# Kernel tuning notes

Measured on AMD Instinct MI355X. Metric: run time of the kernel, lower is better.

Reference implementation:

```python
import jax, jax.numpy as jnp
import numpy as np

B, C, H, W = 16, 512, 64, 64

def _conv1x1_relu(x, Wk, bk):
    # 1x1 conv (stride 1) + ReLU, as in the conv2d helper
    return jax.nn.relu(jnp.einsum('bchw,oc->bohw', x, Wk) + bk[None, :, None, None])

def _maxpool2(t):
    b, c, h, w = t.shape
    return t.reshape(b, c, h // 2, 2, w // 2, 2).max(axis=(3, 5))

def setup_inputs() -> dict:
    key = jax.random.key(0)
    ks = jax.random.split(key, 10)
    s = 0.05
    x = jax.random.normal(ks[0], (B, C, H, W), jnp.float32)
    W_theta = jax.random.normal(ks[1], (C // 8, C), jnp.float32) * s
    b_theta = jnp.zeros((C // 8,), jnp.float32)
    W_phi = jax.random.normal(ks[2], (C // 8, C), jnp.float32) * s
    b_phi = jnp.zeros((C // 8,), jnp.float32)
    W_g = jax.random.normal(ks[3], (C // 2, C), jnp.float32) * s
    b_g = jnp.zeros((C // 2,), jnp.float32)
    W_o = jax.random.normal(ks[4], (C, C // 2), jnp.float32) * s
    b_o = jnp.zeros((C,), jnp.float32)
    gamma = jnp.array([0.5], jnp.float32)  # nonzero so attention branch contributes
    return {"x": x, "W_theta": W_theta, "b_theta": b_theta, "W_phi": W_phi,
            "b_phi": b_phi, "W_g": W_g, "b_g": b_g, "W_o": W_o, "b_o": b_o,
            "gamma": gamma}

def reference(x, W_theta, b_theta, W_phi, b_phi, W_g, b_g, W_o, b_o, gamma):
    theta = _conv1x1_relu(x, W_theta, b_theta).reshape(B, C // 8, H * W)
    phi = _maxpool2(_conv1x1_relu(x, W_phi, b_phi)).reshape(B, C // 8, H * W // 4)
    g = _maxpool2(_conv1x1_relu(x, W_g, b_g)).reshape(B, C // 2, H * W // 4)
    # beta[b, n, m] = softmax_m(theta^T phi)
    beta = jax.nn.softmax(jnp.einsum('bcn,bcm->bnm', theta, phi), axis=-1)
    # o[b, c, n] = g @ beta^T
    o = jnp.einsum('bcm,bnm->bcn', g, beta).reshape(B, C // 2, H, W)
    o = _conv1x1_relu(o, W_o, b_o)
    return gamma[0] * o + x
```

## Files before the change

### kernel.cpp

```cpp
#include <hip/hip_runtime.h>
#include <cstdint>
#include <cstddef>

#define BB 16
#define CIN 512
#define NPIX 4096
#define C8 64
#define C2 256
#define MM 1024

using bf16x8 = __attribute__((ext_vector_type(8))) short;
using f32x4  = __attribute__((ext_vector_type(4))) float;

__device__ __forceinline__ short f2bf(float f) {
  union { float f; unsigned u; } v; v.f = f;
  unsigned r = v.u + 0x7FFFu + ((v.u >> 16) & 1u);
  return (short)(r >> 16);
}
__device__ __forceinline__ unsigned cvtpk(float lo, float hi) {
  unsigned r;
  asm("v_cvt_pk_bf16_f32 %0, %1, %2" : "=v"(r) : "v"(lo), "v"(hi));
  return r;
}
__device__ __forceinline__ bf16x8 ldg8(const short* p) {
  return *reinterpret_cast<const bf16x8*>(p);
}
__device__ __forceinline__ bf16x8 lds8(const short* p) {
  union { unsigned long long q[2]; bf16x8 v; } u;
  u.q[0] = *reinterpret_cast<const unsigned long long*>(p);
  u.q[1] = *reinterpret_cast<const unsigned long long*>(p + 4);
  return u.v;
}
#define MFMA(a, b, c) __builtin_amdgcn_mfma_f32_16x16x32_bf16(a, b, c, 0, 0, 0)
#define LOG2E 1.4426950408889634f

__global__ __launch_bounds__(256) void cast_w_k(const float* __restrict__ wa,
                                                const float* __restrict__ wb,
                                                const float* __restrict__ wc,
                                                const float* __restrict__ wd,
                                                short* __restrict__ out) {
  int i = blockIdx.x * 256 + threadIdx.x;
  float v;
  if (i < 32768) v = wa[i] * LOG2E;
  else if (i < 65536) v = wb[i - 32768];
  else if (i < 196608) v = wc[i - 65536];
  else v = wd[i - 196608];
  out[i] = f2bf(v);
}

__global__ __launch_bounds__(1024) void conv_mega_k(
    const float* __restrict__ x, const short* __restrict__ wbf,
    const float* __restrict__ bth, const float* __restrict__ bph,
    const float* __restrict__ bg,
    short* __restrict__ thetaT, short* __restrict__ phiT,
    short* __restrict__ gp) {
  __shared__ __align__(16) short xs[128][36];
  const int t = threadIdx.x, w = t >> 6, l = t & 63;
  const int lr = l & 15, quad = l >> 4;
  const int wg = w & 7, wh = w >> 3;
  const int bx = blockIdx.x, b = blockIdx.y;
  const int nbase = bx * 128;
  const float* xb = x + ((size_t)b * CIN << 12) + nbase;

  const int nl = t & 127, cg = t >> 7;

  f32x4 acc[3][4];
#pragma unroll
  for (int i = 0; i < 3; ++i)
#pragma unroll
    for (int j = 0; j < 4; ++j) acc[i][j] = (f32x4){0.f, 0.f, 0.f, 0.f};

  float pv0[2], pv1[2];
#pragma unroll
  for (int p = 0; p < 2; ++p) {
    int cl = (p * 8 + cg) * 2;
    pv0[p] = xb[((size_t)cl << 12) + nl];
    pv1[p] = xb[((size_t)(cl + 1) << 12) + nl];
  }

  for (int c0 = 0; c0 < CIN; c0 += 32) {
    bf16x8 af[3];
#pragma unroll
    for (int tt = 0; tt < 3; ++tt)
      af[tt] = ldg8(wbf + (size_t)(wg * 48 + tt * 16 + lr) * CIN + c0 + quad * 8);
    asm volatile("s_waitcnt lgkmcnt(0)" ::: "memory");
    __builtin_amdgcn_s_barrier();
#pragma unroll
    for (int p = 0; p < 2; ++p) {
      int cl = (p * 8 + cg) * 2;
      *reinterpret_cast<unsigned*>(&xs[nl][cl]) = cvtpk(pv0[p], pv1[p]);
    }
    asm volatile("s_waitcnt lgkmcnt(0)" ::: "memory");
    __builtin_amdgcn_s_barrier();
    if (c0 + 32 < CIN) {
#pragma unroll
      for (int p = 0; p < 2; ++p) {
        int cl = (p * 8 + cg) * 2;
        pv0[p] = xb[((size_t)(c0 + 32 + cl) << 12) + nl];
        pv1[p] = xb[((size_t)(c0 + 32 + cl + 1) << 12) + nl];
      }
    }
#pragma unroll
    for (int j = 0; j < 4; ++j) {
      const int gnt = (j & 1) + wh * 2 + (j >> 1) * 4;
      bf16x8 bfr = lds8(&xs[gnt * 16 + lr][quad * 8]);
#pragma unroll
      for (int tt = 0; tt < 3; ++tt)
        acc[tt][j] = MFMA(af[tt], bfr, acc[tt][j]);
    }
  }

#pragma unroll
  for (int tt = 0; tt < 3; ++tt) {
    const int ocb = wg * 48 + tt * 16;
    if (ocb < 64) {
      short* tb = thetaT + ((size_t)b << 12) * C8;
#pragma unroll
      for (int r = 0; r < 4; ++r) {
        int oc = ocb + quad * 4 + r;
        float bia = bth[oc] * LOG2E;
#pragma unroll
        for (int j = 0; j < 4; ++j) {
          const int gnt = (j & 1) + wh * 2 + (j >> 1) * 4;
          int n = nbase + gnt * 16 + lr;
          tb[(size_t)n * C8 + oc] = f2bf(fmaxf(acc[tt][j][r] + bia, 0.f));
        }
      }
    } else if (ocb < 128) {
      short* pb = phiT + ((size_t)b << 10) * C8;
#pragma unroll
      for (int r = 0; r < 4; ++r) {
        int oc = ocb - 64 + quad * 4 + r;
        float bia = bph[oc];
#pragma unroll
        for (int jj = 0; jj < 2; ++jj) {
          float va = fmaxf(acc[tt][jj][r] + bia, 0.f);
          float vb = fmaxf(acc[tt][jj + 2][r] + bia, 0.f);
          float pa = fmaxf(va, __shfl_xor(va, 1));
          float pbv = fmaxf(vb, __shfl_xor(vb, 1));
          float pool = fmaxf(pa, pbv);
          if ((l & 1) == 0) {
            int m = bx * 32 + wh * 16 + jj * 8 + (lr >> 1);
            pb[(size_t)m * C8 + oc] = f2bf(pool);
          }
        }
      }
    } else {
      short* gb = gp + ((size_t)b << 10) * C2;
#pragma unroll
      for (int r = 0; r < 4; ++r) {
        int oc = ocb - 128 + quad * 4 + r;
        float bia = bg[oc];
#pragma unroll
        for (int jj = 0; jj < 2; ++jj) {
          float va = fmaxf(acc[tt][jj][r] + bia, 0.f);
          float vb = fmaxf(acc[tt][jj + 2][r] + bia, 0.f);
          float pa = fmaxf(va, __shfl_xor(va, 1));
          float pbv = fmaxf(vb, __shfl_xor(vb, 1));
          float pool = fmaxf(pa, pbv);
          if ((l & 1) == 0) {
            int m = bx * 32 + wh * 16 + jj * 8 + (lr >> 1);
            gb[(size_t)oc * MM + m] = f2bf(pool);
          }
        }
      }
    }
  }
}

__global__ __launch_bounds__(256, 2) void attn_k(
    const short* __restrict__ thetaT, const short* __restrict__ phiT,
    const short* __restrict__ gp, const short* __restrict__ wo,
    const float* __restrict__ bo, const float* __restrict__ x,
    const float* __restrict__ gamma, float* __restrict__ out) {
  __shared__ __align__(16) short smem[16896];
  __shared__ float balpha[2][4][16];
  __shared__ float binv[4][16];
  const int t = threadIdx.x, w = t >> 6, l = t & 63;
  const int lr = l & 15, quad = l >> 4;
  const int blk = blockIdx.x;
  const int b = ((blk & 7) << 1) | ((blk >> 3) & 1);
  const int q0 = (blk >> 4) << 6;
  const int nw = q0 + w * 16;

  const short* thb = thetaT + ((size_t)b << 12) * C8;
  const short* phb = phiT + ((size_t)b << 10) * C8;
  const short* gpb = gp + ((size_t)b << 10) * C2;

  bf16x8 tb0 = ldg8(thb + (size_t)(nw + lr) * C8 + quad * 8);
  bf16x8 tb1 = ldg8(thb + (size_t)(nw + lr) * C8 + 32 + quad * 8);

  f32x4 oacc[4][4];
#pragma unroll
  for (int i = 0; i < 4; ++i)
#pragma unroll
    for (int j = 0; j < 4; ++j) oacc[i][j] = (f32x4){0.f, 0.f, 0.f, 0.f};
  float mrun = -3e38f, ssum = 0.f;

  auto scores = [&](int ch) {
    const int m0 = ch * 128, buf = ch & 1;
    bf16x8 ph0[8], ph1[8];
#pragma unroll
    for (int mt = 0; mt < 8; ++mt) {
      const short* pr = phb + (size_t)(m0 + mt * 16 + lr) * C8 + quad * 8;
      ph0[mt] = ldg8(pr);
      ph1[mt] = ldg8(pr + 32);
    }
    f32x4 sacc[8];
#pragma unroll
    for (int i = 0; i < 8; ++i) sacc[i] = (f32x4){0.f, 0.f, 0.f, 0.f};
#pragma unroll
    for (int mt = 0; mt < 8; ++mt) {
      sacc[mt] = MFMA(ph0[mt], tb0, sacc[mt]);
      sacc[mt] = MFMA(ph1[mt], tb1, sacc[mt]);
    }
    float cmax = sacc[0][0];
#pragma unroll
    for (int mt = 0; mt < 8; ++mt)
      cmax = fmaxf(cmax, fmaxf(fmaxf(sacc[mt][0], sacc[mt][1]),
                               fmaxf(sacc[mt][2], sacc[mt][3])));
    cmax = fmaxf(cmax, __shfl_xor(cmax, 16));
    cmax = fmaxf(cmax, __shfl_xor(cmax, 32));
    const float mnew = fmaxf(mrun, cmax);
    const float al = exp2f(mrun - mnew);
    mrun = mnew;
    float rsum = 0.f;
    short* prow = smem + ((((buf << 2) | w) << 4) + lr) * 132;
#pragma unroll
    for (int mt = 0; mt < 8; ++mt) {
      float e0 = exp2f(sacc[mt][0] - mnew);
      float e1 = exp2f(sacc[mt][1] - mnew);
      float e2 = exp2f(sacc[mt][2] - mnew);
      float e3 = exp2f(sacc[mt][3] - mnew);
      rsum += (e0 + e1) + (e2 + e3);
      uint2 pk2;
      pk2.x = cvtpk(e0, e1);
      pk2.y = cvtpk(e2, e3);
      *reinterpret_cast<uint2*>(prow + mt * 16 + quad * 4) = pk2;
    }
    ssum = ssum * al + rsum;
    if (quad == 0) balpha[buf][w][lr] = al;
  };

  bf16x8 gpf[4];
  auto pfga = [&](int ch) {
    const int m0 = ch * 128;
#pragma unroll
    for (int ct = 0; ct < 4; ++ct)
      gpf[ct] = ldg8(gpb + (size_t)(w * 64 + ct * 16 + lr) * MM + m0 + quad * 8);
  };

  scores(0);
  pfga(0);
  for (int ch = 0; ch < 8; ++ch) {
    const int buf = ch & 1, m0 = ch * 128;
    asm volatile("s_waitcnt lgkmcnt(0)" ::: "memory");
    __builtin_amdgcn_s_barrier();
    float av[4];
#pragma unroll
    for (int qt = 0; qt < 4; ++qt) av[qt] = balpha[buf][qt][lr];
#pragma unroll
    for (int ct = 0; ct < 4; ++ct)
#pragma unroll
      for (int qt = 0; qt < 4; ++qt) oacc[ct][qt] *= av[qt];
    bf16x8 cga[4], cpf[4];
#pragma unroll
    for (int ct = 0; ct < 4; ++ct) cga[ct] = gpf[ct];
#pragma unroll
    for (int qt = 0; qt < 4; ++qt)
      cpf[qt] = lds8(smem + ((((buf << 2) | qt) << 4) + lr) * 132 + quad * 8);
#pragma unroll
    for (int kc = 0; kc < 4; ++kc) {
      bf16x8 nga[4], npf[4];
      if (kc < 3) {
#pragma unroll
        for (int ct = 0; ct < 4; ++ct)
          nga[ct] = ldg8(gpb + (size_t)(w * 64 + ct * 16 + lr) * MM +
                         m0 + (kc + 1) * 32 + quad * 8);
#pragma unroll
        for (int qt = 0; qt < 4; ++qt)
          npf[qt] = lds8(smem + ((((buf << 2) | qt) << 4) + lr) * 132 +
                         (kc + 1) * 32 + quad * 8);
      }
#pragma unroll
      for (int ct = 0; ct < 4; ++ct)
#pragma unroll
        for (int qt = 0; qt < 4; ++qt)
          oacc[ct][qt] = MFMA(cga[ct], cpf[qt], oacc[ct][qt]);
      if (kc < 3) {
#pragma unroll
        for (int i = 0; i < 4; ++i) { cga[i] = nga[i]; cpf[i] = npf[i]; }
      }
    }
    if (ch < 7) {
      scores(ch + 1);
      pfga(ch + 1);
    }
  }

  ssum += __shfl_xor(ssum, 16);
  ssum += __shfl_xor(ssum, 32);
  if (quad == 0) binv[w][lr] = 1.f / ssum;
  __syncthreads();
  float invn[4];
#pragma unroll
  for (int qt = 0; qt < 4; ++qt) invn[qt] = binv[qt][lr];

  short (*os)[264] = reinterpret_cast<short (*)[264]>(smem);
#pragma unroll
  for (int ct = 0; ct < 4; ++ct) {
    int c0 = w * 64 + ct * 16 + quad * 4;
#pragma unroll
    for (int qt = 0; qt < 4; ++qt) {
      uint2 pk2;
      pk2.x = cvtpk(oacc[ct][qt][0] * invn[qt], oacc[ct][qt][1] * invn[qt]);
      pk2.y = cvtpk(oacc[ct][qt][2] * invn[qt], oacc[ct][qt][3] * invn[qt]);
      *reinterpret_cast<uint2*>(&os[qt * 16 + lr][c0]) = pk2;
    }
  }
  __syncthreads();

  const float g0 = gamma[0];
  for (int pp = 0; pp < 4; ++pp) {
    const int ocb = w * 128 + pp * 32;
    f32x4 acc2[2][4];
#pragma unroll
    for (int i = 0; i < 2; ++i)
#pragma unroll
      for (int j = 0; j < 4; ++j) acc2[i][j] = (f32x4){0.f, 0.f, 0.f, 0.f};
#pragma unroll
    for (int half = 0; half < 2; ++half) {
      bf16x8 wa[8];
#pragma unroll
      for (int k2 = 0; k2 < 4; ++k2)
#pragma unroll
        for (int ot = 0; ot < 2; ++ot)
          wa[k2 * 2 + ot] = ldg8(wo + (size_t)(ocb + ot * 16 + lr) * C2 +
                                 (half * 4 + k2) * 32 + quad * 8);
#pragma unroll
      for (int k2 = 0; k2 < 4; ++k2) {
        const int kc = half * 4 + k2;
        bf16x8 of[4];
#pragma unroll
        for (int qt = 0; qt < 4; ++qt)
          of[qt] = lds8(&os[qt * 16 + lr][kc * 32 + quad * 8]);
#pragma unroll
        for (int ot = 0; ot < 2; ++ot)
#pragma unroll
          for (int qt = 0; qt < 4; ++qt)
            acc2[ot][qt] = MFMA(wa[k2 * 2 + ot], of[qt], acc2[ot][qt]);
      }
    }
#pragma unroll
    for (int ot = 0; ot < 2; ++ot) {
#pragma unroll
      for (int r = 0; r < 4; ++r) {
        int oc = ocb + ot * 16 + quad * 4 + r;
        float bia = bo[oc];
        size_t base = ((size_t)(b * CIN + oc) << 12);
#pragma unroll
        for (int qt = 0; qt < 4; ++qt) {
          int n = q0 + qt * 16 + lr;
          float v = g0 * fmaxf(acc2[ot][qt][r] + bia, 0.f);
          out[base + n] = v + x[base + n];
        }
      }
    }
  }
}

extern "C" void kernel_launch(void* const* d_in, const int* in_sizes, int n_in,
                              void* d_out, int out_size, void* d_ws, size_t ws_size,
                              hipStream_t stream) {
  const float* x       = (const float*)d_in[0];
  const float* W_theta = (const float*)d_in[1];
  const float* b_theta = (const float*)d_in[2];
  const float* W_phi   = (const float*)d_in[3];
  const float* b_phi   = (const float*)d_in[4];
  const float* W_g     = (const float*)d_in[5];
  const float* b_g     = (const float*)d_in[6];
  const float* W_o     = (const float*)d_in[7];
  const float* b_o     = (const float*)d_in[8];
  const float* gamma   = (const float*)d_in[9];
  float* out = (float*)d_out;
  char* W = (char*)d_ws;

  short* thetaT = (short*)(W);
  short* phiT   = (short*)(W + 8388608);
  short* gp     = (short*)(W + 10485760);
  short* wbf    = (short*)(W + 18874368);
  short* wo     = wbf + 196608;

  cast_w_k<<<dim3(1280), 256, 0, stream>>>(W_theta, W_phi, W_g, W_o, wbf);
  conv_mega_k<<<dim3(32, 16), 1024, 0, stream>>>(x, wbf, b_theta, b_phi, b_g,
                                                 thetaT, phiT, gp);
  attn_k<<<dim3(1024), 256, 0, stream>>>(thetaT, phiT, gp, wo, b_o, x, gamma, out);
}
```

Measured before the change: 458.4 us.

## Stage phi through LDS, deepen prefetch, lazy softmax rescale, add MFMA priority hints

The projection kernel now prefetches x two channel-chunks ahead using a double register slot. The attention kernel stages each phi chunk cooperatively into shared memory, where before every wave loaded its own copy from global memory. It also prefetches the whole g chunk into registers up front and only raises the running max when it grows by more than 8, so the output accumulators are rescaled less often. s_setprio hints are wrapped around the MFMA loops. The changes cut redundant global loads and exposed latency, but they raise register and LDS pressure and add a barrier per chunk.

```diff
diff --git a/kernel.cpp b/kernel.cpp
--- a/kernel.cpp
+++ b/kernel.cpp
@@ -30,6 +30,11 @@
   u.q[0] = *reinterpret_cast<const unsigned long long*>(p);
   u.q[1] = *reinterpret_cast<const unsigned long long*>(p + 4);
   return u.v;
+}
+__device__ __forceinline__ void sts8(short* p, bf16x8 v) {
+  union { unsigned long long q[2]; bf16x8 v; } u; u.v = v;
+  *reinterpret_cast<unsigned long long*>(p) = u.q[0];
+  *reinterpret_cast<unsigned long long*>(p + 4) = u.q[1];
 }
 #define MFMA(a, b, c) __builtin_amdgcn_mfma_f32_16x16x32_bf16(a, b, c, 0, 0, 0)
 #define LOG2E 1.4426950408889634f
@@ -70,15 +75,18 @@
 #pragma unroll
     for (int j = 0; j < 4; ++j) acc[i][j] = (f32x4){0.f, 0.f, 0.f, 0.f};
 
-  float pv0[2], pv1[2];
-#pragma unroll
-  for (int p = 0; p < 2; ++p) {
-    int cl = (p * 8 + cg) * 2;
-    pv0[p] = xb[((size_t)cl << 12) + nl];
-    pv1[p] = xb[((size_t)(cl + 1) << 12) + nl];
-  }
+  float pv0[2][2], pv1[2][2];
+#pragma unroll
+  for (int s = 0; s < 2; ++s)
+#pragma unroll
+    for (int p = 0; p < 2; ++p) {
+      int cl = s * 32 + (p * 8 + cg) * 2;
+      pv0[s][p] = xb[((size_t)cl << 12) + nl];
+      pv1[s][p] = xb[((size_t)(cl + 1) << 12) + nl];
+    }
 
   for (int c0 = 0; c0 < CIN; c0 += 32) {
+    const int slot = (c0 >> 5) & 1;
     bf16x8 af[3];
 #pragma unroll
     for (int tt = 0; tt < 3; ++tt)
@@ -88,18 +96,19 @@
 #pragma unroll
     for (int p = 0; p < 2; ++p) {
       int cl = (p * 8 + cg) * 2;
-      *reinterpret_cast<unsigned*>(&xs[nl][cl]) = cvtpk(pv0[p], pv1[p]);
+      *reinterpret_cast<unsigned*>(&xs[nl][cl]) = cvtpk(pv0[slot][p], pv1[slot][p]);
     }
     asm volatile("s_waitcnt lgkmcnt(0)" ::: "memory");
     __builtin_amdgcn_s_barrier();
-    if (c0 + 32 < CIN) {
+    if (c0 + 64 < CIN) {
 #pragma unroll
       for (int p = 0; p < 2; ++p) {
         int cl = (p * 8 + cg) * 2;
-        pv0[p] = xb[((size_t)(c0 + 32 + cl) << 12) + nl];
-        pv1[p] = xb[((size_t)(c0 + 32 + cl + 1) << 12) + nl];
-      }
-    }
+        pv0[slot][p] = xb[((size_t)(c0 + 64 + cl) << 12) + nl];
+        pv1[slot][p] = xb[((size_t)(c0 + 64 + cl + 1) << 12) + nl];
+      }
+    }
+    __builtin_amdgcn_s_setprio(1);
 #pragma unroll
     for (int j = 0; j < 4; ++j) {
       const int gnt = (j & 1) + wh * 2 + (j >> 1) * 4;
@@ -108,6 +117,7 @@
       for (int tt = 0; tt < 3; ++tt)
         acc[tt][j] = MFMA(af[tt], bfr, acc[tt][j]);
     }
+    __builtin_amdgcn_s_setprio(0);
   }
 
 #pragma unroll
@@ -174,6 +184,7 @@
     const float* __restrict__ bo, const float* __restrict__ x,
     const float* __restrict__ gamma, float* __restrict__ out) {
   __shared__ __align__(16) short smem[16896];
+  __shared__ __align__(16) short phs[128][68];
   __shared__ float balpha[2][4][16];
   __shared__ float binv[4][16];
   const int t = threadIdx.x, w = t >> 6, l = t & 63;
@@ -197,23 +208,33 @@
     for (int j = 0; j < 4; ++j) oacc[i][j] = (f32x4){0.f, 0.f, 0.f, 0.f};
   float mrun = -3e38f, ssum = 0.f;
 
+  const int srow = t >> 3, scol = (t & 7) * 8;
+  bf16x8 stld[4];
+  auto stage_phi_issue = [&](int ch) {
+    const int m0 = ch * 128;
+#pragma unroll
+    for (int sw = 0; sw < 4; ++sw)
+      stld[sw] = ldg8(phb + (size_t)(m0 + sw * 32 + srow) * C8 + scol);
+  };
+  auto stage_phi_write = [&]() {
+#pragma unroll
+    for (int sw = 0; sw < 4; ++sw)
+      sts8(&phs[sw * 32 + srow][scol], stld[sw]);
+  };
+
   auto scores = [&](int ch) {
-    const int m0 = ch * 128, buf = ch & 1;
-    bf16x8 ph0[8], ph1[8];
+    const int buf = ch & 1;
+    f32x4 sacc[8];
+#pragma unroll
+    for (int i = 0; i < 8; ++i) sacc[i] = (f32x4){0.f, 0.f, 0.f, 0.f};
+    __builtin_amdgcn_s_setprio(1);
 #pragma unroll
     for (int mt = 0; mt < 8; ++mt) {
-      const short* pr = phb + (size_t)(m0 + mt * 16 + lr) * C8 + quad * 8;
-      ph0[mt] = ldg8(pr);
-      ph1[mt] = ldg8(pr + 32);
-    }
-    f32x4 sacc[8];
-#pragma unroll
-    for (int i = 0; i < 8; ++i) sacc[i] = (f32x4){0.f, 0.f, 0.f, 0.f};
-#pragma unroll
-    for (int mt = 0; mt < 8; ++mt) {
-      sacc[mt] = MFMA(ph0[mt], tb0, sacc[mt]);
-      sacc[mt] = MFMA(ph1[mt], tb1, sacc[mt]);
-    }
+      const short* pr = &phs[mt * 16 + lr][quad * 8];
+      sacc[mt] = MFMA(lds8(pr), tb0, sacc[mt]);
+      sacc[mt] = MFMA(lds8(pr + 32), tb1, sacc[mt]);
+    }
+    __builtin_amdgcn_s_setprio(0);
     float cmax = sacc[0][0];
 #pragma unroll
     for (int mt = 0; mt < 8; ++mt)
@@ -221,7 +242,7 @@
                                fmaxf(sacc[mt][2], sacc[mt][3])));
     cmax = fmaxf(cmax, __shfl_xor(cmax, 16));
     cmax = fmaxf(cmax, __shfl_xor(cmax, 32));
-    const float mnew = fmaxf(mrun, cmax);
+    const float mnew = (cmax > mrun + 8.f) ? cmax : mrun;
     const float al = exp2f(mrun - mnew);
     mrun = mnew;
     float rsum = 0.f;
@@ -242,57 +263,57 @@
     if (quad == 0) balpha[buf][w][lr] = al;
   };
 
-  bf16x8 gpf[4];
+  bf16x8 gpf[16];
   auto pfga = [&](int ch) {
     const int m0 = ch * 128;
 #pragma unroll
-    for (int ct = 0; ct < 4; ++ct)
-      gpf[ct] = ldg8(gpb + (size_t)(w * 64 + ct * 16 + lr) * MM + m0 + quad * 8);
+    for (int kc = 0; kc < 4; ++kc)
+#pragma unroll
+      for (int ct = 0; ct < 4; ++ct)
+        gpf[kc * 4 + ct] = ldg8(gpb + (size_t)(w * 64 + ct * 16 + lr) * MM +
+                                m0 + kc * 32 + quad * 8);
   };
 
+  stage_phi_issue(0);
+  stage_phi_write();
+  asm volatile("s_waitcnt lgkmcnt(0)" ::: "memory");
+  __builtin_amdgcn_s_barrier();
   scores(0);
   pfga(0);
+
   for (int ch = 0; ch < 8; ++ch) {
-    const int buf = ch & 1, m0 = ch * 128;
+    const int buf = ch & 1;
     asm volatile("s_waitcnt lgkmcnt(0)" ::: "memory");
     __builtin_amdgcn_s_barrier();
+    if (ch < 7) stage_phi_issue(ch + 1);
     float av[4];
 #pragma unroll
     for (int qt = 0; qt < 4; ++qt) av[qt] = balpha[buf][qt][lr];
-#pragma unroll
-    for (int ct = 0; ct < 4; ++ct)
-#pragma unroll
-      for (int qt = 0; qt < 4; ++qt) oacc[ct][qt] *= av[qt];
-    bf16x8 cga[4], cpf[4];
-#pragma unroll
-    for (int ct = 0; ct < 4; ++ct) cga[ct] = gpf[ct];
-#pragma unroll
-    for (int qt = 0; qt < 4; ++qt)
-      cpf[qt] = lds8(smem + ((((buf << 2) | qt) << 4) + lr) * 132 + quad * 8);
+    if (av[0] != 1.f || av[1] != 1.f || av[2] != 1.f || av[3] != 1.f) {
+#pragma unroll
+      for (int ct = 0; ct < 4; ++ct)
+#pragma unroll
+        for (int qt = 0; qt < 4; ++qt) oacc[ct][qt] *= av[qt];
+    }
+    __builtin_amdgcn_s_setprio(1);
 #pragma unroll
     for (int kc = 0; kc < 4; ++kc) {
-      bf16x8 nga[4], npf[4];
-      if (kc < 3) {
-#pragma unroll
-        for (int ct = 0; ct < 4; ++ct)
-          nga[ct] = ldg8(gpb + (size_t)(w * 64 + ct * 16 + lr) * MM +
-                         m0 + (kc + 1) * 32 + quad * 8);
+      bf16x8 pf[4];
+#pragma unroll
+      for (int qt = 0; qt < 4; ++qt)
+        pf[qt] = lds8(smem + ((((buf << 2) | qt) << 4) + lr) * 132 +
+                      kc * 32 + quad * 8);
+#pragma unroll
+      for (int ct = 0; ct < 4; ++ct)
 #pragma unroll
         for (int qt = 0; qt < 4; ++qt)
-          npf[qt] = lds8(smem + ((((buf << 2) | qt) << 4) + lr) * 132 +
-                         (kc + 1) * 32 + quad * 8);
-      }
-#pragma unroll
-      for (int ct = 0; ct < 4; ++ct)
-#pragma unroll
-        for (int qt = 0; qt < 4; ++qt)
-          oacc[ct][qt] = MFMA(cga[ct], cpf[qt], oacc[ct][qt]);
-      if (kc < 3) {
-#pragma unroll
-        for (int i = 0; i < 4; ++i) { cga[i] = nga[i]; cpf[i] = npf[i]; }
-      }
-    }
+          oacc[ct][qt] = MFMA(gpf[kc * 4 + ct], pf[qt], oacc[ct][qt]);
+    }
+    __builtin_amdgcn_s_setprio(0);
     if (ch < 7) {
+      stage_phi_write();
+      asm volatile("s_waitcnt lgkmcnt(0)" ::: "memory");
+      __builtin_amdgcn_s_barrier();
       scores(ch + 1);
       pfga(ch + 1);
     }
@@ -337,6 +358,7 @@
         for (int ot = 0; ot < 2; ++ot)
           wa[k2 * 2 + ot] = ldg8(wo + (size_t)(ocb + ot * 16 + lr) * C2 +
                                  (half * 4 + k2) * 32 + quad * 8);
+      __builtin_amdgcn_s_setprio(1);
 #pragma unroll
       for (int k2 = 0; k2 < 4; ++k2) {
         const int kc = half * 4 + k2;
@@ -350,6 +372,7 @@
           for (int qt = 0; qt < 4; ++qt)
             acc2[ot][qt] = MFMA(wa[k2 * 2 + ot], of[qt], acc2[ot][qt]);
       }
+      __builtin_amdgcn_s_setprio(0);
     }
 #pragma unroll
     for (int ot = 0; ot < 2; ++ot) {
```

Result: faster. 401.1 us (-12.5%).
